# Optimization experiments

Hardware: AMD Instinct MI355X
Metric: run time of the kernel (lower is better)

The kernel has to match this reference:

```python
import jax, jax.numpy as jnp
from jax import lax
import numpy as np

V, D, H, K = 50000, 300, 256, 37  # vocab, emb dim, lstm hidden, num_tags
B, T = 64, 256


def setup_inputs() -> dict:
    key = jax.random.key(0)
    ks = jax.random.split(key, 24)
    lengths = jax.random.randint(ks[0], (B,), T // 2, T + 1)
    valid = jnp.arange(T)[None, :] < lengths[:, None]
    text = jnp.where(valid, jax.random.randint(ks[1], (B, T), 1, V), 0)
    sbj = jax.random.randint(ks[2], (B, T), 0, K)

    def p(k, shape, s=0.05):
        return jax.random.normal(k, shape, jnp.float32) * s

    return {
        "text": text, "sbj": sbj,
        "emb": p(ks[3], (V, D), 0.1),
        # layer 0 (input D=300), forward + backward directions, torch gate order i,f,g,o
        "Wih0f": p(ks[4], (4 * H, D)), "Whh0f": p(ks[5], (4 * H, H)), "b0f": jnp.zeros((4 * H,), jnp.float32),
        "Wih0b": p(ks[6], (4 * H, D)), "Whh0b": p(ks[7], (4 * H, H)), "b0b": jnp.zeros((4 * H,), jnp.float32),
        # layer 1 (input 2H=512)
        "Wih1f": p(ks[8], (4 * H, 2 * H)), "Whh1f": p(ks[9], (4 * H, H)), "b1f": jnp.zeros((4 * H,), jnp.float32),
        "Wih1b": p(ks[10], (4 * H, 2 * H)), "Whh1b": p(ks[11], (4 * H, H)), "b1b": jnp.zeros((4 * H,), jnp.float32),
        "W_sbj": p(ks[12], (K, 2 * H)), "b_sbj": jnp.zeros((K,), jnp.float32),
        # CRF params (torchcrf init: uniform(-0.1, 0.1))
        "start_t": p(ks[13], (K,), 0.1), "end_t": p(ks[14], (K,), 0.1), "trans": p(ks[15], (K, K), 0.1),
    }


def _lstm(x, Wih, Whh, b, reverse):
    # x: [T, B, Din] time-major; returns hidden states [T, B, H]
    Bn, Hn = x.shape[1], Whh.shape[1]

    def step(carry, xt):
        h, c = carry
        z = xt @ Wih.T + h @ Whh.T + b
        i, f, g, o = jnp.split(z, 4, axis=-1)
        c = jax.nn.sigmoid(f) * c + jax.nn.sigmoid(i) * jnp.tanh(g)
        h = jax.nn.sigmoid(o) * jnp.tanh(c)
        return (h, c), h

    init = (jnp.zeros((Bn, Hn), x.dtype), jnp.zeros((Bn, Hn), x.dtype))
    return lax.scan(step, init, x, reverse=reverse)[1]


def reference(text, sbj, emb, Wih0f, Whh0f, b0f, Wih0b, Whh0b, b0b,
              Wih1f, Whh1f, b1f, Wih1b, Whh1b, b1b,
              W_sbj, b_sbj, start_t, end_t, trans):
    mask = (text != 0)                      # [B, T]
    x = jnp.transpose(emb[text], (1, 0, 2))  # [T, B, D]
    h0 = jnp.concatenate([_lstm(x, Wih0f, Whh0f, b0f, False),
                          _lstm(x, Wih0b, Whh0b, b0b, True)], axis=-1)   # [T, B, 2H]
    h1 = jnp.concatenate([_lstm(h0, Wih1f, Whh1f, b1f, False),
                          _lstm(h0, Wih1b, Whh1b, b1b, True)], axis=-1)  # [T, B, 2H]
    em = h1 @ W_sbj.T + b_sbj               # emissions [T, B, K]

    tags = sbj.T                            # [T, B]
    m = mask.T                              # [T, B]
    mf = m.astype(em.dtype)

    # --- numerator: score of the gold path ---
    em_sel = jnp.take_along_axis(em, tags[:, :, None], axis=2)[..., 0]  # [T, B]
    tr_sel = trans[tags[:-1], tags[1:]]                                  # [T-1, B]
    seq_ends = m.sum(0) - 1
    last_tags = tags[seq_ends, jnp.arange(tags.shape[1])]
    num = (start_t[tags[0]] + em_sel[0]
           + jnp.sum((em_sel[1:] + tr_sel) * mf[1:], axis=0)
           + end_t[last_tags])              # [B]

    # --- log partition: forward algorithm (logsumexp DP over K tags) ---
    def step(score, inp):
        em_t, m_t = inp
        nxt = jax.scipy.special.logsumexp(
            score[:, :, None] + trans[None, :, :] + em_t[:, None, :], axis=1)
        return jnp.where(m_t[:, None], nxt, score), None

    score0 = start_t[None, :] + em[0]       # [B, K]
    score = lax.scan(step, score0, (em[1:], m[1:]))[0]
    logZ = jax.scipy.special.logsumexp(score + end_t[None, :], axis=-1)  # [B]

    llh = num - logZ
    return -(llh.sum() / mf.sum())          # -1 * token_mean log-likelihood
```

## Files before the change

### kernel.cpp

```cpp
#include <hip/hip_runtime.h>
#include <math.h>

#define TT 256
#define BB 64
#define DD 300
#define KP0 320
#define HH 256
#define KK 37
#define FH 1024
#define MTOT (TT*BB)

typedef __attribute__((ext_vector_type(8))) short short8;
typedef __attribute__((ext_vector_type(4))) float f32x4;

__device__ __forceinline__ float bf2f(unsigned short u) {
    union { float f; unsigned int i; } v; v.i = ((unsigned int)u) << 16; return v.f;
}
__device__ __forceinline__ unsigned short f2bf(float f) {
    union { float f; unsigned int i; } v; v.f = f;
    unsigned int i = v.i;
    unsigned int r = (i + 0x7FFFu + ((i >> 16) & 1u)) >> 16;
    return (unsigned short)r;
}
__device__ __forceinline__ float sigm(float x)   { return 1.0f / (1.0f + __expf(-x)); }
__device__ __forceinline__ float tanh_f(float x) { return 2.0f / (1.0f + __expf(-2.0f * x)) - 1.0f; }

__device__ __forceinline__ int sb0(int w) { return (w << 24) >> 24; }
__device__ __forceinline__ int sb1(int w) { return (w << 16) >> 24; }
__device__ __forceinline__ int sb2(int w) { return (w <<  8) >> 24; }
__device__ __forceinline__ int sb3(int w) { return  w        >> 24; }

#if defined(__has_builtin)
#if __has_builtin(__builtin_amdgcn_sdot4)
#define HAVE_SDOT4 1
#endif
#endif

__device__ __forceinline__ int dot4i8(int a, int b, int c) {
#ifdef HAVE_SDOT4
    return __builtin_amdgcn_sdot4(a, b, c, false);
#else
    return c + sb0(a) * sb0(b) + sb1(a) * sb1(b) + sb2(a) * sb2(b) + sb3(a) * sb3(b);
#endif
}

__device__ __forceinline__ void lstm_dot(int hw, int4 wv, int& a0, int& a1, int& a2, int& a3) {
    a0 = dot4i8(hw, wv.x, a0);
    a1 = dot4i8(hw, wv.y, a1);
    a2 = dot4i8(hw, wv.z, a2);
    a3 = dot4i8(hw, wv.w, a3);
}

__device__ __forceinline__ void barrier_lgkm() {
    asm volatile("s_waitcnt lgkmcnt(0)\n\ts_barrier" ::: "memory");
}

__device__ __forceinline__ int perm_col(int nn) { return ((nn & 255) << 2) | (nn >> 8); }

__global__ __launch_bounds__(64) void conv_quant(
    const float* __restrict__ w0f, const float* __restrict__ w0b,
    const float* __restrict__ w1f, const float* __restrict__ w1b,
    float* __restrict__ S, unsigned int* __restrict__ WQ)
{
    const int m = blockIdx.x >> 10;
    const int r = blockIdx.x & 1023;
    const float* W = m == 0 ? w0f : m == 1 ? w0b : m == 2 ? w1f : w1b;
    const int t = threadIdx.x;
    const float4 wv = *(const float4*)(W + r * HH + t * 4);
    float mx = fmaxf(fmaxf(fabsf(wv.x), fabsf(wv.y)), fmaxf(fabsf(wv.z), fabsf(wv.w)));
    #pragma unroll
    for (int s = 32; s > 0; s >>= 1) mx = fmaxf(mx, __shfl_down(mx, s, 64));
    const float mxall = __shfl(mx, 0, 64);
    const float s = fmaxf(mxall, 1e-20f) / 127.0f;
    const int g = r >> 8, u = r & 255;
    if (t == 0) S[m * 1024 + u * 4 + g] = s;
    int q0 = (int)rintf(wv.x / s), q1 = (int)rintf(wv.y / s);
    int q2 = (int)rintf(wv.z / s), q3 = (int)rintf(wv.w / s);
    q0 = max(-127, min(127, q0)); q1 = max(-127, min(127, q1));
    q2 = max(-127, min(127, q2)); q3 = max(-127, min(127, q3));
    WQ[m * 65536 + (t * 256 + u) * 4 + g] =
        (unsigned int)(q0 & 0xff) | ((unsigned int)(q1 & 0xff) << 8) |
        ((unsigned int)(q2 & 0xff) << 16) | ((unsigned int)(q3 & 0xff) << 24);
}

__global__ __launch_bounds__(256) void conv_wsbj_bf(
    const float* __restrict__ Wsbj, unsigned short* __restrict__ WB)
{
    const int idx = blockIdx.x * 256 + threadIdx.x;
    if (idx >= 64 * 512) return;
    const int r = idx >> 9, cidx = idx & 511;
    WB[idx] = (r < KK) ? f2bf(Wsbj[r * 512 + cidx]) : (unsigned short)0;
}

__global__ __launch_bounds__(320) void conv_gather(
    const int* __restrict__ text, const float* __restrict__ emb,
    unsigned short* __restrict__ Abf)
{
    const int r = blockIdx.x;
    const int k = threadIdx.x;
    const int t = r >> 6, b = r & 63;
    const int idx = text[b * TT + t];
    Abf[r * KP0 + k] = (k < DD) ? f2bf(emb[(size_t)idx * DD + k]) : (unsigned short)0;
}

__global__ __launch_bounds__(256) void conv_w4(
    const float* __restrict__ s0, const float* __restrict__ s1,
    const float* __restrict__ s2, const float* __restrict__ s3,
    unsigned short* __restrict__ d0, unsigned short* __restrict__ d1,
    unsigned short* __restrict__ d2, unsigned short* __restrict__ d3)
{
    const int z = blockIdx.y;
    const float* src = z == 0 ? s0 : z == 1 ? s1 : z == 2 ? s2 : s3;
    unsigned short* dst = z == 0 ? d0 : z == 1 ? d1 : z == 2 ? d2 : d3;
    const int kin   = z < 2 ? DD  : 512;
    const int kout  = z < 2 ? KP0 : 512;
    const int total = 1024 * kout;
    const int idx = blockIdx.x * 256 + threadIdx.x;
    if (idx >= total) return;
    const int rr = idx / kout, k = idx - rr * kout;
    dst[idx] = (k < kin) ? f2bf(src[rr * kin + k]) : (unsigned short)0;
}

__global__ __launch_bounds__(256) void gemm_mfma2(
    const unsigned short* __restrict__ A,
    const unsigned short* __restrict__ Wf,
    const unsigned short* __restrict__ Wb,
    const float* __restrict__ biasf,
    const float* __restrict__ biasb,
    unsigned short* __restrict__ outf,
    unsigned short* __restrict__ outb,
    int lda)
{
    const unsigned short* W = blockIdx.z ? Wb : Wf;
    const float* bias        = blockIdx.z ? biasb : biasf;
    unsigned short* out      = blockIdx.z ? outb : outf;

    const int bm = blockIdx.x * 128;
    const int bn = blockIdx.y * 128;
    const int tid = threadIdx.x;
    const int lane = tid & 63;
    const int wave = tid >> 6;
    const int wm = (wave & 1) * 64;
    const int wn = (wave >> 1) * 64;

    __shared__ __align__(16) unsigned short As[128 * 32];
    __shared__ __align__(16) unsigned short Bs[128 * 32];

    f32x4 acc[4][4] = {};

    const int srow = tid >> 2;
    const int sk = (tid & 3) * 8;

    const unsigned short* ga0 = A + (size_t)(bm + srow) * lda + sk;
    const unsigned short* ga1 = A + (size_t)(bm + srow + 64) * lda + sk;
    const unsigned short* gb0 = W + (size_t)(bn + srow) * lda + sk;
    const unsigned short* gb1 = W + (size_t)(bn + srow + 64) * lda + sk;

    unsigned short* lA0 = As + wave * 512;
    unsigned short* lA1 = As + 2048 + wave * 512;
    unsigned short* lB0 = Bs + wave * 512;
    unsigned short* lB1 = Bs + 2048 + wave * 512;

    const int kiters = lda >> 5;
    for (int kb = 0; kb < kiters; kb++) {
        const int k0 = kb * 32;
        __builtin_amdgcn_global_load_lds(
            (const __attribute__((address_space(1))) unsigned int*)(ga0 + k0),
            (__attribute__((address_space(3))) unsigned int*)lA0, 16, 0, 0);
        __builtin_amdgcn_global_load_lds(
            (const __attribute__((address_space(1))) unsigned int*)(ga1 + k0),
            (__attribute__((address_space(3))) unsigned int*)lA1, 16, 0, 0);
        __builtin_amdgcn_global_load_lds(
            (const __attribute__((address_space(1))) unsigned int*)(gb0 + k0),
            (__attribute__((address_space(3))) unsigned int*)lB0, 16, 0, 0);
        __builtin_amdgcn_global_load_lds(
            (const __attribute__((address_space(1))) unsigned int*)(gb1 + k0),
            (__attribute__((address_space(3))) unsigned int*)lB1, 16, 0, 0);
        __syncthreads();

        short8 af[4], bfr[4];
        #pragma unroll
        for (int i = 0; i < 4; i++) {
            af[i]  = *(const short8*)&As[(wm + i * 16 + (lane & 15)) * 32 + (lane >> 4) * 8];
            bfr[i] = *(const short8*)&Bs[(wn + i * 16 + (lane & 15)) * 32 + (lane >> 4) * 8];
        }
        #pragma unroll
        for (int i = 0; i < 4; i++)
            #pragma unroll
            for (int j = 0; j < 4; j++)
                acc[i][j] = __builtin_amdgcn_mfma_f32_16x16x32_bf16(af[i], bfr[j], acc[i][j], 0, 0, 0);
        __syncthreads();
    }

    const int cn = lane & 15;
    const int cr = (lane >> 4) * 4;
    #pragma unroll
    for (int j = 0; j < 4; j++) {
        const int n = bn + wn + j * 16 + cn;
        const float bv = bias[n];
        const int pc = perm_col(n);
        #pragma unroll
        for (int i = 0; i < 4; i++) {
            #pragma unroll
            for (int r = 0; r < 4; r++) {
                const int m = bm + wm + i * 16 + cr + r;
                out[(size_t)m * FH + pc] = f2bf(acc[i][j][r] + bv);
            }
        }
    }
}

__global__ __launch_bounds__(256) void gemm_em(
    const unsigned short* __restrict__ A,
    const unsigned short* __restrict__ W,
    const float* __restrict__ bias,
    float* __restrict__ em)
{
    const int bm = blockIdx.x * 128;
    const int tid = threadIdx.x;
    const int lane = tid & 63;
    const int wave = tid >> 6;
    const int wm = (wave & 1) * 64;
    const int wn = (wave >> 1) * 32;

    __shared__ __align__(16) unsigned short As[128 * 32];
    __shared__ __align__(16) unsigned short Bs[64 * 32];

    f32x4 acc[4][2] = {};

    const int srow = tid >> 2;
    const int sk = (tid & 3) * 8;

    const unsigned short* ga0 = A + (size_t)(bm + srow) * 512 + sk;
    const unsigned short* ga1 = A + (size_t)(bm + srow + 64) * 512 + sk;
    const unsigned short* gb  = W + (size_t)srow * 512 + sk;

    unsigned short* lA0 = As + wave * 512;
    unsigned short* lA1 = As + 2048 + wave * 512;
    unsigned short* lB  = Bs + wave * 512;

    for (int kb = 0; kb < 16; kb++) {
        const int k0 = kb * 32;
        __builtin_amdgcn_global_load_lds(
            (const __attribute__((address_space(1))) unsigned int*)(ga0 + k0),
            (__attribute__((address_space(3))) unsigned int*)lA0, 16, 0, 0);
        __builtin_amdgcn_global_load_lds(
            (const __attribute__((address_space(1))) unsigned int*)(ga1 + k0),
            (__attribute__((address_space(3))) unsigned int*)lA1, 16, 0, 0);
        __builtin_amdgcn_global_load_lds(
            (const __attribute__((address_space(1))) unsigned int*)(gb + k0),
            (__attribute__((address_space(3))) unsigned int*)lB, 16, 0, 0);
        __syncthreads();

        short8 af[4], bfr[2];
        #pragma unroll
        for (int i = 0; i < 4; i++)
            af[i]  = *(const short8*)&As[(wm + i * 16 + (lane & 15)) * 32 + (lane >> 4) * 8];
        #pragma unroll
        for (int j = 0; j < 2; j++)
            bfr[j] = *(const short8*)&Bs[(wn + j * 16 + (lane & 15)) * 32 + (lane >> 4) * 8];
        #pragma unroll
        for (int i = 0; i < 4; i++)
            #pragma unroll
            for (int j = 0; j < 2; j++)
                acc[i][j] = __builtin_amdgcn_mfma_f32_16x16x32_bf16(af[i], bfr[j], acc[i][j], 0, 0, 0);
        __syncthreads();
    }

    const int cn = lane & 15;
    const int cr = (lane >> 4) * 4;
    #pragma unroll
    for (int j = 0; j < 2; j++) {
        const int n = wn + j * 16 + cn;
        if (n < KK) {
            const float bv = bias[n];
            #pragma unroll
            for (int i = 0; i < 4; i++) {
                #pragma unroll
                for (int r = 0; r < 4; r++) {
                    const int m = bm + wm + i * 16 + cr + r;
                    em[(size_t)m * KK + n] = acc[i][j][r] + bv;
                }
            }
        }
    }
}

__global__ __launch_bounds__(512, 2) void lstm_kernel(
    const unsigned short* __restrict__ zin_f, const unsigned short* __restrict__ zin_b,
    const int* __restrict__ WQf, const int* __restrict__ WQb,
    const float* __restrict__ Sf, const float* __restrict__ Sb,
    unsigned short* __restrict__ h_out)
{
    const int dir = blockIdx.y;
    const unsigned short* zin = dir ? zin_b : zin_f;
    const int*   WQ = dir ? WQb : WQf;
    const float* S  = dir ? Sb  : Sf;
    const int off = dir ? HH : 0;

    const int b = blockIdx.x;
    const int tid = threadIdx.x;
    const int u  = tid & 255;
    const int kh = tid >> 8;

    __shared__ __align__(16) unsigned char hq8[2][HH];
    __shared__ int4 red[HH];

    const int4* wp = (const int4*)WQ + kh * 32 * 256 + u;
    int4 w[32];
    #pragma unroll
    for (int j = 0; j < 32; j++) w[j] = wp[j * 256];

    float4 sc = make_float4(0.f, 0.f, 0.f, 0.f);
    if (kh == 0) {
        sc = *(const float4*)(S + 4 * u);
        const float inv127 = 1.0f / 127.0f;
        sc.x *= inv127; sc.y *= inv127; sc.z *= inv127; sc.w *= inv127;
    }
    float c = 0.0f;
    int cur = 0;
    if (tid < 128) ((unsigned int*)hq8)[tid] = 0u;
    __syncthreads();

    ushort4 zv = make_ushort4(0, 0, 0, 0);
    if (kh == 0) {
        const int tt0 = dir ? (TT - 1) : 0;
        zv = *(const ushort4*)(zin + (tt0 * BB + b) * FH + 4 * u);
    }

    for (int ts = 0; ts < TT; ts++) {
        const int tt = dir ? (TT - 1 - ts) : ts;
        const int row = tt * BB + b;

        ushort4 zv_n = make_ushort4(0, 0, 0, 0);
        if (kh == 0) {
            const int ts_n = (ts + 1 < TT) ? (ts + 1) : ts;
            const int tt_n = dir ? (TT - 1 - ts_n) : ts_n;
            zv_n = *(const ushort4*)(zin + (tt_n * BB + b) * FH + 4 * u);
        }

        const int4* hv = (const int4*)&hq8[cur][kh * 128];
        int a0 = 0, a1 = 0, a2 = 0, a3 = 0;
        #pragma unroll
        for (int jq = 0; jq < 8; jq++) {
            const int4 hw = hv[jq];
            lstm_dot(hw.x, w[4 * jq + 0], a0, a1, a2, a3);
            lstm_dot(hw.y, w[4 * jq + 1], a0, a1, a2, a3);
            lstm_dot(hw.z, w[4 * jq + 2], a0, a1, a2, a3);
            lstm_dot(hw.w, w[4 * jq + 3], a0, a1, a2, a3);
        }

        if (kh) red[u] = make_int4(a0, a1, a2, a3);
        barrier_lgkm();

        if (kh == 0) {
            const int4 r0 = red[u];
            const int A0 = a0 + r0.x;
            const int A1 = a1 + r0.y;
            const int A2 = a2 + r0.z;
            const int A3 = a3 + r0.w;
            const float zi  = (float)A0 * sc.x + bf2f(zv.x);
            const float zf_ = (float)A1 * sc.y + bf2f(zv.y);
            const float zg  = (float)A2 * sc.z + bf2f(zv.z);
            const float zo  = (float)A3 * sc.w + bf2f(zv.w);
            const float cc = sigm(zf_) * c + sigm(zi) * tanh_f(zg);
            c = cc;
            const float hh = sigm(zo) * tanh_f(cc);
            hq8[cur ^ 1][u] = (unsigned char)((int)rintf(hh * 127.0f));
            h_out[row * (2 * HH) + off + u] = f2bf(hh);
        }
        barrier_lgkm();
        cur ^= 1;
        zv = zv_n;
    }
}

__global__ __launch_bounds__(64) void crf_kernel(
    const int* __restrict__ text, const int* __restrict__ sbj,
    const float* __restrict__ em,
    const float* __restrict__ start_t, const float* __restrict__ end_t,
    const float* __restrict__ trans, float* __restrict__ accum)
{
    const int b = blockIdx.x;
    const int tid = threadIdx.x;
    __shared__ float tr[KK * KK];
    __shared__ float sc[2][KK];
    for (int x = tid; x < KK * KK; x += 64) tr[x] = trans[x];

    int cnt = 0;
    for (int t = tid; t < TT; t += 64) cnt += (text[b * TT + t] != 0) ? 1 : 0;
    #pragma unroll
    for (int s = 32; s > 0; s >>= 1) cnt += __shfl_down(cnt, s, 64);
    const int len = __shfl(cnt, 0, 64);

    __syncthreads();

    float part = 0.f;
    for (int t = tid; t < TT; t += 64) {
        if (t >= 1 && t < len) {
            const int tg = sbj[b * TT + t];
            const int tp = sbj[b * TT + t - 1];
            part += em[(t * BB + b) * KK + tg] + tr[tp * KK + tg];
        }
    }
    #pragma unroll
    for (int s = 32; s > 0; s >>= 1) part += __shfl_down(part, s, 64);

    float tc[KK];
    #pragma unroll
    for (int k1 = 0; k1 < KK; k1++) tc[k1] = (tid < KK) ? tr[k1 * KK + tid] : 0.f;

    if (tid < KK) sc[0][tid] = start_t[tid] + em[b * KK + tid];
    __syncthreads();
    int cur = 0;
    float ev = (tid < KK && len > 1) ? em[(BB + b) * KK + tid] : 0.f;
    for (int t = 1; t < len; t++) {
        const float ev_n = (tid < KK && t + 1 < len) ? em[((t + 1) * BB + b) * KK + tid] : 0.f;
        float nv = 0.f;
        if (tid < KK) {
            float v[KK];
            float mx = -1e30f;
            #pragma unroll
            for (int k1 = 0; k1 < KK; k1++) {
                v[k1] = sc[cur][k1] + tc[k1];
                mx = fmaxf(mx, v[k1]);
            }
            float s = 0.f;
            #pragma unroll
            for (int k1 = 0; k1 < KK; k1++)
                s += __expf(v[k1] - mx);
            nv = mx + __logf(s) + ev;
        }
        if (tid < KK) sc[cur ^ 1][tid] = nv;
        barrier_lgkm();
        cur ^= 1;
        ev = ev_n;
    }

    if (tid == 0) {
        const int tg0 = sbj[b * TT];
        const int tgl = sbj[b * TT + len - 1];
        const float num = start_t[tg0] + em[b * KK + tg0] + part + end_t[tgl];
        float mx = -1e30f;
        for (int k = 0; k < KK; k++) mx = fmaxf(mx, sc[cur][k] + end_t[k]);
        float s = 0.f;
        for (int k = 0; k < KK; k++) s += __expf(sc[cur][k] + end_t[k] - mx);
        const float logZ = mx + __logf(s);
        atomicAdd(&accum[0], num - logZ);
        atomicAdd(&accum[1], (float)len);
    }
}

__global__ void init_kernel(float* __restrict__ accum) {
    if (threadIdx.x < 2) accum[threadIdx.x] = 0.0f;
}
__global__ void final_kernel(const float* __restrict__ accum, float* __restrict__ out) {
    out[0] = -(accum[0] / accum[1]);
}

extern "C" void kernel_launch(void* const* d_in, const int* in_sizes, int n_in,
                              void* d_out, int out_size, void* d_ws, size_t ws_size,
                              hipStream_t stream)
{
    (void)in_sizes; (void)n_in; (void)out_size; (void)ws_size;
    const int*   text  = (const int*)d_in[0];
    const int*   sbj   = (const int*)d_in[1];
    const float* emb   = (const float*)d_in[2];
    const float* Wih0f = (const float*)d_in[3];
    const float* Whh0f = (const float*)d_in[4];
    const float* b0f   = (const float*)d_in[5];
    const float* Wih0b = (const float*)d_in[6];
    const float* Whh0b = (const float*)d_in[7];
    const float* b0b   = (const float*)d_in[8];
    const float* Wih1f = (const float*)d_in[9];
    const float* Whh1f = (const float*)d_in[10];
    const float* b1f   = (const float*)d_in[11];
    const float* Wih1b = (const float*)d_in[12];
    const float* Whh1b = (const float*)d_in[13];
    const float* b1b   = (const float*)d_in[14];
    const float* Wsbj  = (const float*)d_in[15];
    const float* bsbj  = (const float*)d_in[16];
    const float* start_t = (const float*)d_in[17];
    const float* end_t   = (const float*)d_in[18];
    const float* trans   = (const float*)d_in[19];

    char* ws = (char*)d_ws;
    unsigned short* zf   = (unsigned short*)(ws + 0);
    unsigned short* zb   = (unsigned short*)(ws + 33554432);
    unsigned short* h0   = (unsigned short*)(ws + 67108864);
    unsigned short* h1   = (unsigned short*)(ws + 83886080);
    unsigned short* Wb0f = (unsigned short*)(ws + 67108864);
    unsigned short* Wb0b = (unsigned short*)(ws + 67764224);
    unsigned short* Abf  = (unsigned short*)(ws + 83886080);
    unsigned short* Wb1f = (unsigned short*)(ws + 94371840);
    unsigned short* Wb1b = (unsigned short*)(ws + 95420416);
    unsigned int*   WQ   = (unsigned int*)(ws + 100663296);
    float*          Sq   = (float*)(ws + 101711872);
    unsigned short* WsbjB = (unsigned short*)(ws + 102760448);
    float*          acc  = (float*)(ws + 102836224);
    float*           em  = (float*)(ws + 0);
    float* out = (float*)d_out;

    const int* WQ0f = (const int*)(WQ + 0 * 65536);
    const int* WQ0b = (const int*)(WQ + 1 * 65536);
    const int* WQ1f = (const int*)(WQ + 2 * 65536);
    const int* WQ1b = (const int*)(WQ + 3 * 65536);
    const float* S0f = Sq + 0 * 1024;
    const float* S0b = Sq + 1 * 1024;
    const float* S1f = Sq + 2 * 1024;
    const float* S1b = Sq + 3 * 1024;

    init_kernel<<<1, 64, 0, stream>>>(acc);
    conv_quant<<<dim3(4096), 64, 0, stream>>>(Whh0f, Whh0b, Whh1f, Whh1b, Sq, WQ);
    conv_wsbj_bf<<<dim3(128), 256, 0, stream>>>(Wsbj, WsbjB);
    conv_gather<<<dim3(MTOT), 320, 0, stream>>>(text, emb, Abf);
    conv_w4<<<dim3(2048, 4), 256, 0, stream>>>(Wih0f, Wih0b, Wih1f, Wih1b,
                                               Wb0f, Wb0b, Wb1f, Wb1b);

    gemm_mfma2<<<dim3(128, 8, 2), 256, 0, stream>>>(Abf, Wb0f, Wb0b, b0f, b0b, zf, zb, KP0);
    lstm_kernel<<<dim3(BB, 2), 512, 0, stream>>>(zf, zb, WQ0f, WQ0b, S0f, S0b, h0);
    gemm_mfma2<<<dim3(128, 8, 2), 256, 0, stream>>>(h0, Wb1f, Wb1b, b1f, b1b, zf, zb, 512);
    lstm_kernel<<<dim3(BB, 2), 512, 0, stream>>>(zf, zb, WQ1f, WQ1b, S1f, S1b, h1);

    gemm_em<<<dim3(128), 256, 0, stream>>>(h1, WsbjB, bsbj, em);
    crf_kernel<<<BB, 64, 0, stream>>>(text, sbj, em, start_t, end_t, trans, acc);
    final_kernel<<<1, 1, 0, stream>>>(acc, out);
}
```

Before: 972.1 us.

## Process two batch rows per LSTM block, streaming weights from memory

Each LSTM block now handles two batch rows instead of one, halving the grid to 64 blocks. The weight slice is no longer held in 32 int4 registers; it is reloaded from global memory (likely L2-resident) at every timestep and shared by both rows' dot products. This cuts register pressure and the number of blocks, but each step of the serial recurrence now waits on global weight loads and does twice the dot-product work.

```diff
diff --git a/kernel.cpp b/kernel.cpp
--- a/kernel.cpp
+++ b/kernel.cpp
@@ -298,18 +298,16 @@
     const float* S  = dir ? Sb  : Sf;
     const int off = dir ? HH : 0;
 
-    const int b = blockIdx.x;
+    const int b0 = blockIdx.x * 2;
+    const int b1 = b0 + 1;
     const int tid = threadIdx.x;
     const int u  = tid & 255;
     const int kh = tid >> 8;
 
-    __shared__ __align__(16) unsigned char hq8[2][HH];
-    __shared__ int4 red[HH];
+    __shared__ __align__(16) unsigned char hq8[2][2][HH];
+    __shared__ int4 red[2][HH];
 
     const int4* wp = (const int4*)WQ + kh * 32 * 256 + u;
-    int4 w[32];
-    #pragma unroll
-    for (int j = 0; j < 32; j++) w[j] = wp[j * 256];
 
     float4 sc = make_float4(0.f, 0.f, 0.f, 0.f);
     if (kh == 0) {
@@ -317,61 +315,92 @@
         const float inv127 = 1.0f / 127.0f;
         sc.x *= inv127; sc.y *= inv127; sc.z *= inv127; sc.w *= inv127;
     }
-    float c = 0.0f;
+    float c0 = 0.0f, c1 = 0.0f;
     int cur = 0;
-    if (tid < 128) ((unsigned int*)hq8)[tid] = 0u;
+    if (tid < 256) ((unsigned int*)hq8)[tid] = 0u;
     __syncthreads();
 
-    ushort4 zv = make_ushort4(0, 0, 0, 0);
+    ushort4 zv0 = make_ushort4(0, 0, 0, 0), zv1 = zv0;
     if (kh == 0) {
         const int tt0 = dir ? (TT - 1) : 0;
-        zv = *(const ushort4*)(zin + (tt0 * BB + b) * FH + 4 * u);
+        zv0 = *(const ushort4*)(zin + (tt0 * BB + b0) * FH + 4 * u);
+        zv1 = *(const ushort4*)(zin + (tt0 * BB + b1) * FH + 4 * u);
     }
 
     for (int ts = 0; ts < TT; ts++) {
         const int tt = dir ? (TT - 1 - ts) : ts;
-        const int row = tt * BB + b;
-
-        ushort4 zv_n = make_ushort4(0, 0, 0, 0);
+        const int row = tt * BB;
+
+        ushort4 zv0_n = make_ushort4(0, 0, 0, 0), zv1_n = zv0_n;
         if (kh == 0) {
             const int ts_n = (ts + 1 < TT) ? (ts + 1) : ts;
             const int tt_n = dir ? (TT - 1 - ts_n) : ts_n;
-            zv_n = *(const ushort4*)(zin + (tt_n * BB + b) * FH + 4 * u);
-        }
-
-        const int4* hv = (const int4*)&hq8[cur][kh * 128];
+            zv0_n = *(const ushort4*)(zin + (tt_n * BB + b0) * FH + 4 * u);
+            zv1_n = *(const ushort4*)(zin + (tt_n * BB + b1) * FH + 4 * u);
+        }
+
+        const int4* hv0 = (const int4*)&hq8[cur][0][kh * 128];
+        const int4* hv1 = (const int4*)&hq8[cur][1][kh * 128];
         int a0 = 0, a1 = 0, a2 = 0, a3 = 0;
+        int d0 = 0, d1 = 0, d2 = 0, d3 = 0;
         #pragma unroll
         for (int jq = 0; jq < 8; jq++) {
-            const int4 hw = hv[jq];
-            lstm_dot(hw.x, w[4 * jq + 0], a0, a1, a2, a3);
-            lstm_dot(hw.y, w[4 * jq + 1], a0, a1, a2, a3);
-            lstm_dot(hw.z, w[4 * jq + 2], a0, a1, a2, a3);
-            lstm_dot(hw.w, w[4 * jq + 3], a0, a1, a2, a3);
-        }
-
-        if (kh) red[u] = make_int4(a0, a1, a2, a3);
+            const int4 hw0 = hv0[jq];
+            const int4 hw1 = hv1[jq];
+            {
+                const int4 wv = wp[(4 * jq + 0) * 256];
+                lstm_dot(hw0.x, wv, a0, a1, a2, a3);
+                lstm_dot(hw1.x, wv, d0, d1, d2, d3);
+            }
+            {
+                const int4 wv = wp[(4 * jq + 1) * 256];
+                lstm_dot(hw0.y, wv, a0, a1, a2, a3);
+                lstm_dot(hw1.y, wv, d0, d1, d2, d3);
+            }
+            {
+                const int4 wv = wp[(4 * jq + 2) * 256];
+                lstm_dot(hw0.z, wv, a0, a1, a2, a3);
+                lstm_dot(hw1.z, wv, d0, d1, d2, d3);
+            }
+            {
+                const int4 wv = wp[(4 * jq + 3) * 256];
+                lstm_dot(hw0.w, wv, a0, a1, a2, a3);
+                lstm_dot(hw1.w, wv, d0, d1, d2, d3);
+            }
+        }
+
+        if (kh) {
+            red[0][u] = make_int4(a0, a1, a2, a3);
+            red[1][u] = make_int4(d0, d1, d2, d3);
+        }
         barrier_lgkm();
 
         if (kh == 0) {
-            const int4 r0 = red[u];
-            const int A0 = a0 + r0.x;
-            const int A1 = a1 + r0.y;
-            const int A2 = a2 + r0.z;
-            const int A3 = a3 + r0.w;
-            const float zi  = (float)A0 * sc.x + bf2f(zv.x);
-            const float zf_ = (float)A1 * sc.y + bf2f(zv.y);
-            const float zg  = (float)A2 * sc.z + bf2f(zv.z);
-            const float zo  = (float)A3 * sc.w + bf2f(zv.w);
-            const float cc = sigm(zf_) * c + sigm(zi) * tanh_f(zg);
-            c = cc;
-            const float hh = sigm(zo) * tanh_f(cc);
-            hq8[cur ^ 1][u] = (unsigned char)((int)rintf(hh * 127.0f));
-            h_out[row * (2 * HH) + off + u] = f2bf(hh);
+            const int4 r0 = red[0][u];
+            const int4 r1 = red[1][u];
+            const int A0 = a0 + r0.x, A1 = a1 + r0.y, A2 = a2 + r0.z, A3 = a3 + r0.w;
+            const int D0 = d0 + r1.x, D1 = d1 + r1.y, D2 = d2 + r1.z, D3 = d3 + r1.w;
+            const float zi0 = (float)A0 * sc.x + bf2f(zv0.x);
+            const float zf0 = (float)A1 * sc.y + bf2f(zv0.y);
+            const float zg0 = (float)A2 * sc.z + bf2f(zv0.z);
+            const float zo0 = (float)A3 * sc.w + bf2f(zv0.w);
+            const float zi1 = (float)D0 * sc.x + bf2f(zv1.x);
+            const float zf1 = (float)D1 * sc.y + bf2f(zv1.y);
+            const float zg1 = (float)D2 * sc.z + bf2f(zv1.z);
+            const float zo1 = (float)D3 * sc.w + bf2f(zv1.w);
+            const float cc0 = sigm(zf0) * c0 + sigm(zi0) * tanh_f(zg0);
+            const float cc1 = sigm(zf1) * c1 + sigm(zi1) * tanh_f(zg1);
+            c0 = cc0; c1 = cc1;
+            const float hh0 = sigm(zo0) * tanh_f(cc0);
+            const float hh1 = sigm(zo1) * tanh_f(cc1);
+            hq8[cur ^ 1][0][u] = (unsigned char)((int)rintf(hh0 * 127.0f));
+            hq8[cur ^ 1][1][u] = (unsigned char)((int)rintf(hh1 * 127.0f));
+            h_out[(row + b0) * (2 * HH) + off + u] = f2bf(hh0);
+            h_out[(row + b1) * (2 * HH) + off + u] = f2bf(hh1);
         }
         barrier_lgkm();
         cur ^= 1;
-        zv = zv_n;
+        zv0 = zv0_n; zv1 = zv1_n;
     }
 }
 
@@ -518,9 +547,9 @@
                                                Wb0f, Wb0b, Wb1f, Wb1b);
 
     gemm_mfma2<<<dim3(128, 8, 2), 256, 0, stream>>>(Abf, Wb0f, Wb0b, b0f, b0b, zf, zb, KP0);
-    lstm_kernel<<<dim3(BB, 2), 512, 0, stream>>>(zf, zb, WQ0f, WQ0b, S0f, S0b, h0);
+    lstm_kernel<<<dim3(BB / 2, 2), 512, 0, stream>>>(zf, zb, WQ0f, WQ0b, S0f, S0b, h0);
     gemm_mfma2<<<dim3(128, 8, 2), 256, 0, stream>>>(h0, Wb1f, Wb1b, b1f, b1b, zf, zb, 512);
-    lstm_kernel<<<dim3(BB, 2), 512, 0, stream>>>(zf, zb, WQ1f, WQ1b, S1f, S1b, h1);
+    lstm_kernel<<<dim3(BB / 2, 2), 512, 0, stream>>>(zf, zb, WQ1f, WQ1b, S1f, S1b, h1);
 
     gemm_em<<<dim3(128), 256, 0, stream>>>(h1, WsbjB, bsbj, em);
     crf_kernel<<<BB, 64, 0, stream>>>(text, sbj, em, start_t, end_t, trans, acc);
```

New measurement: 1.384 ms. 1.42x slower.
